# Performance work log

Hardware: AMD Instinct MI355X
Metric: run time of the kernel (lower is better)

Reference implementation:

```python
import jax, jax.numpy as jnp
import numpy as np

KN = 2048       # 12*N spatio-temporal tokens
B = 4           # batch
D_MODEL = 512
N_HEADS = 8
HEAD_DIM = D_MODEL // N_HEADS
FACTOR = 5
U_PART = min(FACTOR * int(np.ceil(np.log(KN))), KN)  # sample_k == n_top == 40


def setup_inputs() -> dict:
    rng = jax.random.key(0)
    ks = jax.random.split(rng, 12)
    d = D_MODEL
    wscale = 1.0 / np.sqrt(d)  # xavier-ish init scale
    return {
        "query": jax.random.normal(ks[0], (KN, B, d), jnp.float32),
        "key": jax.random.normal(ks[1], (KN, B, d), jnp.float32),
        "value": jax.random.normal(ks[2], (KN, B, d), jnp.float32),
        "index_sample": jax.random.randint(ks[3], (KN, U_PART), 0, KN),
        "Wq": jax.random.normal(ks[4], (d, d), jnp.float32) * wscale,
        "bq": jnp.zeros((d,), jnp.float32),
        "Wk": jax.random.normal(ks[5], (d, d), jnp.float32) * wscale,
        "bk": jnp.zeros((d,), jnp.float32),
        "Wv": jax.random.normal(ks[6], (d, d), jnp.float32) * wscale,
        "bv": jnp.zeros((d,), jnp.float32),
        "Wo": jax.random.normal(ks[7], (d, d), jnp.float32) * wscale,
        "bo": jnp.zeros((d,), jnp.float32),
    }


def reference(query, key, value, index_sample, Wq, bq, Wk, bk, Wv, bv, Wo, bo):
    kN, Bb, d = query.shape
    H, E = N_HEADS, HEAD_DIM
    scaling = E ** -0.5

    # projections (torch Linear: x @ W.T + b); q is scaled before reshaping
    q = (query @ Wq.T + bq) * scaling
    k = key @ Wk.T + bk
    v = value @ Wv.T + bv

    # [kN, B, d] -> [B, H, kN, E]
    def to_bhne(x):
        return x.reshape(kN, Bb, H, E).transpose(1, 2, 0, 3)

    Q, K, V = to_bhne(q), to_bhne(k), to_bhne(v)

    # ProbSparse: sample U_PART keys per query row (shared index table)
    K_samp = K[:, :, index_sample, :]                       # [B,H,kN,S,E]
    QK_samp = jnp.einsum('bhne,bhnse->bhns', Q, K_samp)      # [B,H,kN,S]
    # sparsity measure M = max - mean(over full kN, as in source)
    M = QK_samp.max(axis=-1) - QK_samp.sum(axis=-1) / kN     # [B,H,kN]
    _, M_top = jax.lax.top_k(M, U_PART)                      # [B,H,S]

    # reduced queries attend over ALL keys
    Q_red = jnp.take_along_axis(Q, M_top[..., None], axis=2)  # [B,H,S,E]
    scores = jnp.einsum('bhse,bhne->bhsn', Q_red, K)          # [B,H,S,kN]
    attn = jax.nn.softmax(scores, axis=-1)
    upd = jnp.einsum('bhsn,bhne->bhse', attn, V)              # [B,H,S,E]

    # initial context = mean(V) broadcast; scatter-update the top rows
    ctx = jnp.broadcast_to(V.mean(axis=2, keepdims=True), V.shape)  # [B,H,kN,E]
    bi = jnp.arange(Bb)[:, None, None]
    hi = jnp.arange(H)[None, :, None]
    ctx = ctx.at[bi, hi, M_top].set(upd)

    out = ctx.transpose(0, 2, 1, 3).reshape(Bb, kN, d) @ Wo.T + bo  # [B,kN,d]
    return out
```

## Files before the change

### kernel.cpp

```cpp
#include <hip/hip_runtime.h>
#include <hip/hip_bf16.h>

#define KN 2048
#define BB 4
#define DM 512
#define NH 8
#define HE 64
#define UP 40
#define NBH 32
#define NROWS 8192
#define MiB(x) ((size_t)(x) << 20)

typedef __attribute__((ext_vector_type(8))) short short8;
typedef __attribute__((ext_vector_type(4))) float f32x4;

__device__ __forceinline__ ushort f2bf(float x) {
  unsigned u = __float_as_uint(x);
  unsigned r = (u + 0x7FFFu + ((u >> 16) & 1u)) >> 16;
  return (ushort)r;
}
__device__ __forceinline__ float bf2f(ushort h) {
  return __uint_as_float((unsigned)h << 16);
}

__global__ __launch_bounds__(256) void wsplit3_kernel(
    const float* __restrict__ W0, const float* __restrict__ W1,
    const float* __restrict__ W2, ushort* __restrict__ Wh,
    ushort* __restrict__ Wl) {
  const int which = blockIdx.x >> 9;
  const float* W = (which == 0) ? W0 : (which == 1) ? W1 : W2;
  size_t base = (size_t)which * 262144;
  int i = ((blockIdx.x & 511) * 256 + threadIdx.x) * 2;
  float2 v = *(const float2*)(W + i);
  ushort h0 = f2bf(v.x), h1 = f2bf(v.y);
  ushort l0 = f2bf(v.x - bf2f(h0)), l1 = f2bf(v.y - bf2f(h1));
  *(ushort2*)(Wh + base + i) = make_ushort2(h0, h1);
  *(ushort2*)(Wl + base + i) = make_ushort2(l0, l1);
}

#define APAD 40
__global__ __launch_bounds__(256) void gemm3_mfma(
    const float* __restrict__ A0, const float* __restrict__ A1,
    const float* __restrict__ A2,
    const ushort* __restrict__ Wh3, const ushort* __restrict__ Wl3,
    const float* __restrict__ bq, const float* __restrict__ bk,
    const float* __restrict__ bv, float* __restrict__ QKV) {
  __shared__ ushort AsH[64 * APAD];
  __shared__ ushort AsL[64 * APAD];
  __shared__ ushort WsH[256 * APAD];
  __shared__ ushort WsL[256 * APAD];

  const int which = blockIdx.x >> 8;
  const int local = blockIdx.x & 255;
  const int xcd = local & 7;
  const int idx = local >> 3;
  const int ot = idx >> 4;
  const int mt = xcd * 16 + (idx & 15);
  const int m0 = mt * 64, o0 = ot * 256;

  const float* A = (which == 0) ? A0 : (which == 1) ? A1 : A2;
  const ushort* Wh = Wh3 + (size_t)which * 262144;
  const ushort* Wl = Wl3 + (size_t)which * 262144;
  const float* bias = (which == 0) ? bq : (which == 1) ? bk : bv;
  float* C = QKV + (size_t)which * 8192 * 512;
  const float scale = (which == 0) ? 0.125f : 1.0f;

  const int tid = threadIdx.x;
  const int w = tid >> 6, lane = tid & 63;
  const int fr = lane & 15;
  const int kc = lane >> 4;

  f32x4 acc[4][4];
#pragma unroll
  for (int i = 0; i < 4; ++i)
#pragma unroll
    for (int j = 0; j < 4; ++j)
#pragma unroll
      for (int r = 0; r < 4; ++r) acc[i][j][r] = 0.f;

  for (int k0 = 0; k0 < 512; k0 += 32) {
#pragma unroll
    for (int i = 0; i < 2; ++i) {
      int c = tid + i * 256;
      int row = c >> 3, q = c & 7;
      float4 v = *(const float4*)(A + (size_t)(m0 + row) * 512 + k0 + q * 4);
      ushort h0 = f2bf(v.x), h1 = f2bf(v.y), h2 = f2bf(v.z), h3 = f2bf(v.w);
      ushort l0 = f2bf(v.x - bf2f(h0)), l1 = f2bf(v.y - bf2f(h1));
      ushort l2 = f2bf(v.z - bf2f(h2)), l3 = f2bf(v.w - bf2f(h3));
      *(ushort4*)(AsH + row * APAD + q * 4) = make_ushort4(h0, h1, h2, h3);
      *(ushort4*)(AsL + row * APAD + q * 4) = make_ushort4(l0, l1, l2, l3);
    }
#pragma unroll
    for (int i = 0; i < 4; ++i) {
      int c = tid + i * 256;
      int row = c >> 2, kq = (c & 3) * 8;
      size_t gw = (size_t)(o0 + row) * 512 + k0 + kq;
      int lo = row * APAD + kq;
      *(short8*)(WsH + lo) = *(const short8*)(Wh + gw);
      *(short8*)(WsL + lo) = *(const short8*)(Wl + gw);
    }
    __syncthreads();

    short8 ah[4], al[4], bh[4], bl[4];
#pragma unroll
    for (int i = 0; i < 4; ++i) {
      int off = (i * 16 + fr) * APAD + kc * 8;
      ah[i] = *(const short8*)(AsH + off);
      al[i] = *(const short8*)(AsL + off);
    }
#pragma unroll
    for (int j = 0; j < 4; ++j) {
      int off = (w * 64 + j * 16 + fr) * APAD + kc * 8;
      bh[j] = *(const short8*)(WsH + off);
      bl[j] = *(const short8*)(WsL + off);
    }
#pragma unroll
    for (int i = 0; i < 4; ++i)
#pragma unroll
      for (int j = 0; j < 4; ++j) {
        acc[i][j] = __builtin_amdgcn_mfma_f32_16x16x32_bf16(
            ah[i], bh[j], acc[i][j], 0, 0, 0);
        acc[i][j] = __builtin_amdgcn_mfma_f32_16x16x32_bf16(
            ah[i], bl[j], acc[i][j], 0, 0, 0);
        acc[i][j] = __builtin_amdgcn_mfma_f32_16x16x32_bf16(
            al[i], bh[j], acc[i][j], 0, 0, 0);
      }
    __syncthreads();
  }

#pragma unroll
  for (int i = 0; i < 4; ++i)
#pragma unroll
    for (int j = 0; j < 4; ++j)
#pragma unroll
      for (int r = 0; r < 4; ++r) {
        int m = m0 + i * 16 + (lane >> 4) * 4 + r;
        int o = o0 + w * 64 + j * 16 + fr;
        C[(size_t)m * 512 + o] = (acc[i][j][r] + bias[o]) * scale;
      }
}

__global__ __launch_bounds__(256) void transposeK_kernel(
    const float* __restrict__ K, float* __restrict__ Kt) {
  const int bh = blockIdx.x & 31;
  const int nt = blockIdx.x >> 5;
  const int b = bh >> 3, h = bh & 7;
  const int n0 = nt * 128;
  const int tid = threadIdx.x;
  __shared__ float T[128][65];

#pragma unroll
  for (int i = 0; i < 8; ++i) {
    int flat = tid + i * 256;
    int r = flat >> 4;
    int c4 = flat & 15;
    float4 v = *(const float4*)(K + (((size_t)(n0 + r) * 4 + b) * 8 + h) * 64 + c4 * 4);
    T[r][c4 * 4 + 0] = v.x; T[r][c4 * 4 + 1] = v.y;
    T[r][c4 * 4 + 2] = v.z; T[r][c4 * 4 + 3] = v.w;
  }
  __syncthreads();

  const int nl = tid & 127;
  const int eg = tid >> 7;
#pragma unroll
  for (int e = eg * 32; e < eg * 32 + 32; ++e)
    Kt[((size_t)bh * 64 + e) * 2048 + n0 + nl] = T[nl][e];
}

__global__ __launch_bounds__(256) void mscore_kernel(
    const float* __restrict__ Q, const float* __restrict__ K,
    const int* __restrict__ idx, float* __restrict__ Mout) {
  const int bh = blockIdx.x & 31;
  const int c  = blockIdx.x >> 5;
  const int wv = threadIdx.x >> 6;
  const int lane = threadIdx.x & 63;
  const int n = c * 4 + wv;
  const int b = bh >> 3, h = bh & 7;
  const int g = lane >> 4;
  const int e16 = lane & 15;

  const float4 qv = *(const float4*)(Q + (((size_t)n * 4 + b) * 8 + h) * 64 + e16 * 4);

  float mx = -INFINITY, sm = 0.f;
#pragma unroll
  for (int it = 0; it < 10; ++it) {
    const int s = it * 4 + g;
    const int kn = idx[n * UP + s];
    const float4 kv = *(const float4*)(K + (((size_t)kn * 4 + b) * 8 + h) * 64 + e16 * 4);
    float d = qv.x * kv.x + qv.y * kv.y + qv.z * kv.z + qv.w * kv.w;
    d += __shfl_xor(d, 1);
    d += __shfl_xor(d, 2);
    d += __shfl_xor(d, 4);
    d += __shfl_xor(d, 8);
    mx = fmaxf(mx, d);
    sm += d;
  }
  mx = fmaxf(mx, __shfl_xor(mx, 16));
  mx = fmaxf(mx, __shfl_xor(mx, 32));
  sm += __shfl_xor(sm, 16);
  sm += __shfl_xor(sm, 32);
  if (lane == 0) Mout[(size_t)bh * 2048 + n] = mx - sm * (1.0f / (float)KN);
}

__global__ __launch_bounds__(256) void topk_kernel(
    const float* __restrict__ M, int* __restrict__ Mtop) {
  const int bh = blockIdx.x;
  __shared__ unsigned keys[2048];
  __shared__ int hist[256];
  __shared__ int suf[256];
  __shared__ int scal[2];
  __shared__ int ties[128];
  __shared__ int cnts[2];

  const int tid = threadIdx.x;
  const float* Mrow = M + (size_t)bh * 2048;
#pragma unroll
  for (int i = 0; i < 8; ++i) {
    int j = tid + i * 256;
    unsigned u = __float_as_uint(Mrow[j]);
    keys[j] = (u & 0x80000000u) ? ~u : (u | 0x80000000u);
  }
  if (tid < 2) cnts[tid] = 0;

  unsigned prefix = 0, prefmask = 0;
  int rank = UP;
#pragma unroll
  for (int shift = 24; shift >= 0; shift -= 8) {
    hist[tid] = 0;
    __syncthreads();
#pragma unroll
    for (int i = 0; i < 8; ++i) {
      unsigned k = keys[tid + i * 256];
      if ((k & prefmask) == prefix)
        atomicAdd(&hist[(k >> shift) & 0xFFu], 1);
    }
    __syncthreads();
    suf[tid] = hist[tid];
    __syncthreads();
#pragma unroll
    for (int off = 1; off < 256; off <<= 1) {
      int add = (tid + off < 256) ? suf[tid + off] : 0;
      __syncthreads();
      suf[tid] += add;
      __syncthreads();
    }
    {
      int above = suf[tid] - hist[tid];
      if (above < rank && rank <= suf[tid]) {
        scal[0] = tid;
        scal[1] = rank - above;
      }
    }
    __syncthreads();
    prefix |= ((unsigned)scal[0]) << shift;
    prefmask |= 0xFFu << shift;
    rank = scal[1];
    __syncthreads();
  }
  const unsigned T = prefix;

#pragma unroll
  for (int i = 0; i < 8; ++i) {
    int j = tid + i * 256;
    unsigned k = keys[j];
    if (k > T) {
      int p = atomicAdd(&cnts[0], 1);
      Mtop[bh * UP + p] = j;
    } else if (k == T) {
      int p = atomicAdd(&cnts[1], 1);
      if (p < 128) ties[p] = j;
    }
  }
  __syncthreads();
  if (tid == 0) {
    int base = cnts[0];
    int need = UP - base;
    int tc = cnts[1] < 128 ? cnts[1] : 128;
    for (int s = 0; s < need; ++s) {
      int best = 1 << 30, bj = 0;
      for (int j = 0; j < tc; ++j) {
        int v = ties[j];
        if (v < best) { best = v; bj = j; }
      }
      Mtop[bh * UP + base + s] = best;
      ties[bj] = 1 << 30;
    }
  }
}

__global__ __launch_bounds__(256) void meanv_part(
    const float* __restrict__ V, float* __restrict__ part) {
  const int rc = blockIdx.x >> 3;
  const int cc = blockIdx.x & 7;
  const int c = cc * 256 + threadIdx.x;
  const float* p = V + (size_t)rc * 64 * 2048 + c;
  float acc = 0.f;
#pragma unroll 8
  for (int i = 0; i < 64; ++i) acc += p[(size_t)i * 2048];
  part[(size_t)rc * 2048 + c] = acc;
}

__global__ __launch_bounds__(256) void meanv_final(
    const float* __restrict__ part, float* __restrict__ mnV) {
  const int c = blockIdx.x * 256 + threadIdx.x;
  float acc = 0.f;
#pragma unroll
  for (int r = 0; r < 32; ++r) acc += part[(size_t)r * 2048 + c];
  mnV[c] = acc * (1.0f / (float)KN);
}

__global__ __launch_bounds__(256) void meanout_kernel(
    const float* __restrict__ mnV, const float* __restrict__ Wo,
    const float* __restrict__ bo, float* __restrict__ mo) {
  const int b = blockIdx.x >> 3;
  const int oc = blockIdx.x & 7;
  const int ol = threadIdx.x & 63;
  const int kp = threadIdx.x >> 6;
  const int o = oc * 64 + ol;
  __shared__ float red[4][64];

  const float* m = mnV + b * 512;
  const float* w = Wo + (size_t)o * 512;
  float acc = 0.f;
#pragma unroll 8
  for (int k = kp * 128; k < kp * 128 + 128; ++k)
    acc = fmaf(m[k], w[k], acc);
  red[kp][ol] = acc;
  __syncthreads();
  if (threadIdx.x < 64) {
    float s = red[0][ol] + red[1][ol] + red[2][ol] + red[3][ol];
    mo[b * 512 + o] = s + bo[o];
  }
}

__global__ void fillout_kernel(const float* __restrict__ mo,
                               float* __restrict__ out) {
  size_t i = ((size_t)blockIdx.x * 256 + threadIdx.x) * 4;
  int d = (int)(i & 511);
  int b = (int)(i >> 20);
  float4 v = *(const float4*)(mo + (b << 9) + d);
  *(float4*)(out + i) = v;
}

__global__ __launch_bounds__(128) void fillsel_kernel(
    const int* __restrict__ Mtop, const float* __restrict__ mnV,
    float* __restrict__ ctx) {
  const int i = blockIdx.x;
  const int b = (i / UP) >> 3;
  const int row = b * 2048 + Mtop[i];
  float4 v = *(const float4*)(mnV + b * 512 + threadIdx.x * 4);
  *(float4*)(ctx + (size_t)row * 512 + threadIdx.x * 4) = v;
}

__global__ __launch_bounds__(256) void gemm_rows(
    const float* __restrict__ ctx, const float* __restrict__ W,
    const float* __restrict__ bias, const int* __restrict__ Mtop,
    float* __restrict__ out) {
  __shared__ float As[32][36];
  __shared__ float Ws[32][68];
  __shared__ int rsel[32];
  const int rt = blockIdx.x >> 3;
  const int ot = blockIdx.x & 7;
  const int o0 = ot * 64;
  const int tid = threadIdx.x;
  const int tx = tid & 15;
  const int ty = tid >> 4;

  if (tid < 32) {
    int g = rt * 32 + tid;
    int b = (g / UP) >> 3;
    rsel[tid] = b * 2048 + Mtop[g];
  }
  __syncthreads();

  float acc[2][4] = {};
  for (int k0 = 0; k0 < 512; k0 += 32) {
    {
      int row = tid >> 3, q = tid & 7;
      float4 av = *(const float4*)(ctx + (size_t)rsel[row] * 512 + k0 + q * 4);
      As[q * 4 + 0][row] = av.x; As[q * 4 + 1][row] = av.y;
      As[q * 4 + 2][row] = av.z; As[q * 4 + 3][row] = av.w;
    }
#pragma unroll
    for (int i = 0; i < 2; ++i) {
      int flat = tid + i * 256;
      int r = flat >> 3, q = flat & 7;
      float4 wv = *(const float4*)(W + (size_t)(o0 + r) * 512 + k0 + q * 4);
      Ws[q * 4 + 0][r] = wv.x; Ws[q * 4 + 1][r] = wv.y;
      Ws[q * 4 + 2][r] = wv.z; Ws[q * 4 + 3][r] = wv.w;
    }
    __syncthreads();
#pragma unroll
    for (int kk = 0; kk < 32; ++kk) {
      float a_[2], w_[4];
#pragma unroll
      for (int i = 0; i < 2; ++i) a_[i] = As[kk][ty * 2 + i];
#pragma unroll
      for (int j = 0; j < 4; ++j) w_[j] = Ws[kk][tx * 4 + j];
#pragma unroll
      for (int i = 0; i < 2; ++i)
#pragma unroll
        for (int j = 0; j < 4; ++j)
          acc[i][j] = fmaf(a_[i], w_[j], acc[i][j]);
    }
    __syncthreads();
  }

#pragma unroll
  for (int i = 0; i < 2; ++i) {
    int m = rsel[ty * 2 + i];
#pragma unroll
    for (int j = 0; j < 4; ++j) {
      int o = o0 + tx * 4 + j;
      out[(size_t)m * 512 + o] = acc[i][j] + bias[o];
    }
  }
}

#define QG 5
#define NC 4
__global__ __launch_bounds__(256) void attn_part(
    const float* __restrict__ Q, const float* __restrict__ Kt,
    const float* __restrict__ V, const int* __restrict__ Mtop,
    float* __restrict__ pmax, float* __restrict__ psum,
    float* __restrict__ pvp) {
  const int bh = blockIdx.x & 31;
  const int t  = blockIdx.x >> 5;
  const int g  = t & 7;
  const int ch = t >> 3;
  const int b = bh >> 3, h = bh & 7;
  const int tid = threadIdx.x;
  const int wv = tid >> 6, lane = tid & 63;
  const int n0 = ch * 512;

  __shared__ float qs[QG][64];
  __shared__ float p[QG][512];
  __shared__ float redm[QG][4];
  __shared__ float reds[QG][4];
  __shared__ float pvs[4][QG][64];

  for (int i = tid; i < QG * 64; i += 256) {
    int q = i >> 6, e = i & 63;
    int nq = Mtop[bh * UP + g * QG + q];
    qs[q][e] = Q[(((size_t)nq * 4 + b) * 8 + h) * 64 + e];
  }
  __syncthreads();

  const float* ktb = Kt + (size_t)bh * 64 * 2048;
  float d0[QG] = {}, d1[QG] = {};
  const int nb = n0 + tid * 2;
  for (int e = 0; e < 64; ++e) {
    float2 kv = *(const float2*)(ktb + (size_t)e * 2048 + nb);
#pragma unroll
    for (int q = 0; q < QG; ++q) {
      float qe = qs[q][e];
      d0[q] = fmaf(qe, kv.x, d0[q]);
      d1[q] = fmaf(qe, kv.y, d1[q]);
    }
  }

#pragma unroll
  for (int q = 0; q < QG; ++q) {
    float m_ = fmaxf(d0[q], d1[q]);
#pragma unroll
    for (int off = 1; off < 64; off <<= 1)
      m_ = fmaxf(m_, __shfl_xor(m_, off));
    if (lane == 0) redm[q][wv] = m_;
  }
  __syncthreads();
  float gm[QG];
#pragma unroll
  for (int q = 0; q < QG; ++q)
    gm[q] = fmaxf(fmaxf(redm[q][0], redm[q][1]),
                  fmaxf(redm[q][2], redm[q][3]));

  float ls[QG];
#pragma unroll
  for (int q = 0; q < QG; ++q) {
    float e0 = __expf(d0[q] - gm[q]);
    float e1 = __expf(d1[q] - gm[q]);
    p[q][tid * 2] = e0;
    p[q][tid * 2 + 1] = e1;
    ls[q] = e0 + e1;
  }
#pragma unroll
  for (int q = 0; q < QG; ++q) {
    float s_ = ls[q];
#pragma unroll
    for (int off = 1; off < 64; off <<= 1)
      s_ += __shfl_xor(s_, off);
    if (lane == 0) reds[q][wv] = s_;
  }
  __syncthreads();
  float den[QG];
#pragma unroll
  for (int q = 0; q < QG; ++q)
    den[q] = reds[q][0] + reds[q][1] + reds[q][2] + reds[q][3];

  float acc[QG] = {};
  for (int nn = wv * 128; nn < wv * 128 + 128; ++nn) {
    float v = V[(((size_t)(n0 + nn) * 4 + b) * 8 + h) * 64 + lane];
#pragma unroll
    for (int q = 0; q < QG; ++q) acc[q] = fmaf(p[q][nn], v, acc[q]);
  }
#pragma unroll
  for (int q = 0; q < QG; ++q) pvs[wv][q][lane] = acc[q];
  __syncthreads();

  for (int i = tid; i < QG * 64; i += 256) {
    int q = i >> 6, e = i & 63;
    int slot = bh * UP + g * QG + q;
    float pv = pvs[0][q][e] + pvs[1][q][e] + pvs[2][q][e] + pvs[3][q][e];
    pvp[((size_t)slot * NC + ch) * 64 + e] = pv;
    if (e == 0) {
      pmax[slot * NC + ch] = gm[q];
      psum[slot * NC + ch] = den[q];
    }
  }
}

__global__ __launch_bounds__(64) void attn_combine(
    const float* __restrict__ pmax, const float* __restrict__ psum,
    const float* __restrict__ pvp, float* __restrict__ upd) {
  const int slot = blockIdx.x;
  const int e = threadIdx.x;
  float m = -INFINITY;
#pragma unroll
  for (int ch = 0; ch < NC; ++ch) m = fmaxf(m, pmax[slot * NC + ch]);
  float den = 0.f, num = 0.f;
#pragma unroll
  for (int ch = 0; ch < NC; ++ch) {
    float w = __expf(pmax[slot * NC + ch] - m);
    den = fmaf(w, psum[slot * NC + ch], den);
    num = fmaf(w, pvp[((size_t)slot * NC + ch) * 64 + e], num);
  }
  upd[(size_t)slot * 64 + e] = num / den;
}

__global__ void scatter_kernel(const float* __restrict__ upd,
                               const int* __restrict__ Mtop,
                               float* __restrict__ ctx) {
  const int blk = blockIdx.x;
  const int bh = blk / UP;
  const int b = bh >> 3, h = bh & 7;
  const int n = Mtop[blk];
  ctx[((size_t)(b * 2048 + n)) * 512 + h * 64 + threadIdx.x] =
      upd[(size_t)blk * 64 + threadIdx.x];
}

extern "C" void kernel_launch(void* const* d_in, const int* in_sizes, int n_in,
                              void* d_out, int out_size, void* d_ws,
                              size_t ws_size, hipStream_t stream) {
  const float* query = (const float*)d_in[0];
  const float* key   = (const float*)d_in[1];
  const float* value = (const float*)d_in[2];
  const int*   idxs  = (const int*)d_in[3];
  const float* Wq = (const float*)d_in[4];
  const float* bq = (const float*)d_in[5];
  const float* Wk = (const float*)d_in[6];
  const float* bk = (const float*)d_in[7];
  const float* Wv = (const float*)d_in[8];
  const float* bv = (const float*)d_in[9];
  const float* Wo = (const float*)d_in[10];
  const float* bo = (const float*)d_in[11];
  float* out = (float*)d_out;

  char* ws = (char*)d_ws;
  float*  Mbuf  = (float*)(ws + 0);
  float*  upd   = (float*)(ws + 262144);
  float*  mnV   = (float*)(ws + 589824);
  int*    Mtop  = (int*)  (ws + 598016);
  float*  vpart = (float*)(ws + 634880);
  float*  mo    = (float*)(ws + 941312);
  float*  QKV   = (float*)(ws + MiB(1));
  float*  Q     = QKV;
  float*  K     = (float*)(ws + MiB(17));
  float*  V     = (float*)(ws + MiB(33));
  float*  Kt    = (float*)(ws + MiB(49));
  ushort* Wh3   = (ushort*)(ws + MiB(65));
  ushort* Wl3   = (ushort*)(ws + MiB(65) + 1572864);
  float*  pmax  = (float*)(ws + MiB(68));
  float*  psum  = (float*)(ws + MiB(68) + 32768);
  float*  pvp   = (float*)(ws + MiB(68) + 65536);
  float*  ctx   = Q;

  wsplit3_kernel<<<1536, 256, 0, stream>>>(Wq, Wk, Wv, Wh3, Wl3);
  gemm3_mfma<<<768, 256, 0, stream>>>(query, key, value, Wh3, Wl3,
                                      bq, bk, bv, QKV);

  transposeK_kernel<<<512, 256, 0, stream>>>(K, Kt);

  mscore_kernel<<<16384, 256, 0, stream>>>(Q, K, idxs, Mbuf);
  topk_kernel<<<NBH, 256, 0, stream>>>(Mbuf, Mtop);

  meanv_part<<<256, 256, 0, stream>>>(V, vpart);
  meanv_final<<<8, 256, 0, stream>>>(vpart, mnV);

  attn_part<<<NBH * 32, 256, 0, stream>>>(Q, Kt, V, Mtop, pmax, psum, pvp);
  attn_combine<<<NBH * UP, 64, 0, stream>>>(pmax, psum, pvp, upd);

  fillsel_kernel<<<NBH * UP, 128, 0, stream>>>(Mtop, mnV, ctx);
  scatter_kernel<<<NBH * UP, 64, 0, stream>>>(upd, Mtop, ctx);

  meanout_kernel<<<32, 256, 0, stream>>>(mnV, Wo, bo, mo);
  fillout_kernel<<<4096, 256, 0, stream>>>(mo, out);
  gemm_rows<<<320, 256, 0, stream>>>(ctx, Wo, bo, Mtop, out);
}
```

Baseline: 189.1 us.

## Double-buffer A tile in LDS and load W fragments directly from global

```diff
diff --git a/kernel.cpp b/kernel.cpp
--- a/kernel.cpp
+++ b/kernel.cpp
@@ -45,10 +45,8 @@
     const ushort* __restrict__ Wh3, const ushort* __restrict__ Wl3,
     const float* __restrict__ bq, const float* __restrict__ bk,
     const float* __restrict__ bv, float* __restrict__ QKV) {
-  __shared__ ushort AsH[64 * APAD];
-  __shared__ ushort AsL[64 * APAD];
-  __shared__ ushort WsH[256 * APAD];
-  __shared__ ushort WsL[256 * APAD];
+  __shared__ ushort AsH[2][64 * APAD];
+  __shared__ ushort AsL[2][64 * APAD];
 
   const int which = blockIdx.x >> 8;
   const int local = blockIdx.x & 255;
@@ -78,41 +76,46 @@
 #pragma unroll
       for (int r = 0; r < 4; ++r) acc[i][j][r] = 0.f;
 
-  for (int k0 = 0; k0 < 512; k0 += 32) {
-#pragma unroll
-    for (int i = 0; i < 2; ++i) {
-      int c = tid + i * 256;
-      int row = c >> 3, q = c & 7;
-      float4 v = *(const float4*)(A + (size_t)(m0 + row) * 512 + k0 + q * 4);
-      ushort h0 = f2bf(v.x), h1 = f2bf(v.y), h2 = f2bf(v.z), h3 = f2bf(v.w);
-      ushort l0 = f2bf(v.x - bf2f(h0)), l1 = f2bf(v.y - bf2f(h1));
-      ushort l2 = f2bf(v.z - bf2f(h2)), l3 = f2bf(v.w - bf2f(h3));
-      *(ushort4*)(AsH + row * APAD + q * 4) = make_ushort4(h0, h1, h2, h3);
-      *(ushort4*)(AsL + row * APAD + q * 4) = make_ushort4(l0, l1, l2, l3);
-    }
-#pragma unroll
-    for (int i = 0; i < 4; ++i) {
-      int c = tid + i * 256;
-      int row = c >> 2, kq = (c & 3) * 8;
-      size_t gw = (size_t)(o0 + row) * 512 + k0 + kq;
-      int lo = row * APAD + kq;
-      *(short8*)(WsH + lo) = *(const short8*)(Wh + gw);
-      *(short8*)(WsL + lo) = *(const short8*)(Wl + gw);
-    }
-    __syncthreads();
+  const int srow0 = tid >> 3, sq0 = tid & 7;
+  const int srow1 = (tid + 256) >> 3, sq1 = (tid + 256) & 7;
+
+#define STAGE_A(BUF, K0)                                                    \
+  do {                                                                      \
+    float4 v0 = *(const float4*)(A + (size_t)(m0 + srow0) * 512 + (K0) + sq0 * 4); \
+    float4 v1 = *(const float4*)(A + (size_t)(m0 + srow1) * 512 + (K0) + sq1 * 4); \
+    ushort h0 = f2bf(v0.x), h1 = f2bf(v0.y), h2 = f2bf(v0.z), h3 = f2bf(v0.w); \
+    *(ushort4*)(&AsH[BUF][srow0 * APAD + sq0 * 4]) = make_ushort4(h0, h1, h2, h3); \
+    *(ushort4*)(&AsL[BUF][srow0 * APAD + sq0 * 4]) = make_ushort4(           \
+        f2bf(v0.x - bf2f(h0)), f2bf(v0.y - bf2f(h1)),                        \
+        f2bf(v0.z - bf2f(h2)), f2bf(v0.w - bf2f(h3)));                       \
+    ushort g0 = f2bf(v1.x), g1 = f2bf(v1.y), g2 = f2bf(v1.z), g3 = f2bf(v1.w); \
+    *(ushort4*)(&AsH[BUF][srow1 * APAD + sq1 * 4]) = make_ushort4(g0, g1, g2, g3); \
+    *(ushort4*)(&AsL[BUF][srow1 * APAD + sq1 * 4]) = make_ushort4(           \
+        f2bf(v1.x - bf2f(g0)), f2bf(v1.y - bf2f(g1)),                        \
+        f2bf(v1.z - bf2f(g2)), f2bf(v1.w - bf2f(g3)));                       \
+  } while (0)
+
+  STAGE_A(0, 0);
+
+#pragma unroll
+  for (int it = 0; it < 16; ++it) {
+    const int cur = it & 1;
+    const int k0 = it * 32;
+    __syncthreads();
+    if (it + 1 < 16) STAGE_A(!cur ? 1 : 0, k0 + 32);
 
     short8 ah[4], al[4], bh[4], bl[4];
 #pragma unroll
     for (int i = 0; i < 4; ++i) {
       int off = (i * 16 + fr) * APAD + kc * 8;
-      ah[i] = *(const short8*)(AsH + off);
-      al[i] = *(const short8*)(AsL + off);
+      ah[i] = *(const short8*)(&AsH[cur][off]);
+      al[i] = *(const short8*)(&AsL[cur][off]);
     }
 #pragma unroll
     for (int j = 0; j < 4; ++j) {
-      int off = (w * 64 + j * 16 + fr) * APAD + kc * 8;
-      bh[j] = *(const short8*)(WsH + off);
-      bl[j] = *(const short8*)(WsL + off);
+      size_t off = (size_t)(o0 + w * 64 + j * 16 + fr) * 512 + k0 + kc * 8;
+      bh[j] = *(const short8*)(Wh + off);
+      bl[j] = *(const short8*)(Wl + off);
     }
 #pragma unroll
     for (int i = 0; i < 4; ++i)
@@ -125,7 +128,6 @@
         acc[i][j] = __builtin_amdgcn_mfma_f32_16x16x32_bf16(
             al[i], bh[j], acc[i][j], 0, 0, 0);
       }
-    __syncthreads();
   }
 
 #pragma unroll
```

Measured after the change: 188.2 us. No clear change (-0.5%).
